# Optimization experiments

Measured on AMD Instinct MI355X. Metric: run time of the kernel, lower is better.

## Reference

```python
import jax, jax.numpy as jnp
import numpy as np


def setup_inputs() -> dict:
    key = jax.random.key(0)
    ks = jax.random.split(key, 4)
    B, C, H, W = 8, 512, 128, 128
    K, D = 150, 512
    std = 0.02
    return {
        "x": jax.random.normal(ks[0], (B, C, H, W), dtype=jnp.float32),
        "cls_repr": jax.random.normal(ks[1], (1, K, D), dtype=jnp.float32) * std,
        "W_cls": jax.random.normal(ks[2], (D, D), dtype=jnp.float32) * std,
        "W_feat": jax.random.normal(ks[3], (D, D), dtype=jnp.float32) * std,
        "ln_gamma": jnp.ones((K,), dtype=jnp.float32),
        "ln_beta": jnp.zeros((K,), dtype=jnp.float32),
    }


def reference(x, cls_repr, W_cls, W_feat, ln_gamma, ln_beta):
    b, c, h, w = x.shape
    K = cls_repr.shape[1]
    # img_feat: [b, hw, c]
    img_feat = jnp.transpose(x, (0, 2, 3, 1)).reshape(b, h * w, c)
    cls = jnp.broadcast_to(cls_repr, (b, K, c))
    # coupled_attn: [b, K, hw]
    coupled_attn = jnp.einsum("bnc,bkc->bkn", img_feat, cls)
    # class-direction softmax over hw, feeds class offsets
    cls_attn = jax.nn.softmax(coupled_attn, axis=2)                 # [b,K,hw]
    cls_offset = jnp.einsum("bkn,bnc->bkc", cls_attn, img_feat) @ W_cls.T
    aligned_cls = cls + cls_offset                                   # [b,K,c]
    # position-direction softmax over K, feeds feature offsets
    pos_attn = jax.nn.softmax(coupled_attn, axis=1)                 # [b,K,hw]
    feat_offset = jnp.einsum("bkn,bkc->bnc", pos_attn, cls) @ W_feat.T
    aligned_feat = img_feat + feat_offset                            # [b,hw,c]
    # masks: [b, hw, K], LayerNorm over K
    masks = jnp.einsum("bnc,bkc->bnk", aligned_feat, aligned_cls)
    mu = jnp.mean(masks, axis=-1, keepdims=True)
    var = jnp.var(masks, axis=-1, keepdims=True)
    masks = (masks - mu) * jax.lax.rsqrt(var + 1e-5) * ln_gamma + ln_beta
    return jnp.transpose(masks, (0, 2, 1)).reshape(b, K, h, w)
```

## Files before the change

### kernel.cpp

```cpp
#include <hip/hip_runtime.h>
#include <math.h>

#define BB 8
#define CC 512
#define HWN 16384
#define KK 150
#define KP 160
#define NSEG 16
#define SEGN (HWN / NSEG)

typedef short bf8v __attribute__((ext_vector_type(8)));
typedef float f4v __attribute__((ext_vector_type(4)));

static __device__ inline unsigned short f2b(float f) {
  unsigned u = __float_as_uint(f);
  u += 0x7fffu + ((u >> 16) & 1u);
  return (unsigned short)(u >> 16);
}
static __device__ inline float b2f(unsigned short s) {
  return __uint_as_float(((unsigned)s) << 16);
}
static __device__ inline float b2fs(short s) { return b2f((unsigned short)s); }

typedef const __attribute__((address_space(1))) void* gas_p;
typedef __attribute__((address_space(3))) void* las_p;
static __device__ __forceinline__ void gload16(const void* gp, void* lp) {
  __builtin_amdgcn_global_load_lds((gas_p)gp, (las_p)lp, 16, 0, 0);
}

__global__ __launch_bounds__(256) void t0_prep(const float* __restrict__ cls,
                                               const float* __restrict__ Wc,
                                               const float* __restrict__ Wf,
                                               unsigned short* __restrict__ cls16,
                                               unsigned short* __restrict__ Wc16,
                                               unsigned short* __restrict__ Wf16,
                                               unsigned short* __restrict__ MT16,
                                               unsigned short* __restrict__ AC16) {
  int i = blockIdx.x * 256 + threadIdx.x;
  if (i < KP * CC) {
    int k = i >> 9, c = i & 511;
    cls16[i] = (k < KK) ? f2b(cls[k * CC + c]) : 0;
  }
  if (i < BB * KP * KP) MT16[i] = 0;
  if (i < BB * (KP - KK) * CC) {
    int b = i / ((KP - KK) * CC);
    int r = i % ((KP - KK) * CC);
    int k = KK + (r >> 9);
    int c = r & 511;
    AC16[((size_t)b * KP + k) * CC + c] = 0;
  }
  if (i < CC * CC) {
    Wc16[i] = f2b(Wc[i]);
    Wf16[i] = f2b(Wf[i]);
  }
}

__global__ __launch_bounds__(256) void t1_transpose(const float* __restrict__ x,
                                                    unsigned short* __restrict__ xT,
                                                    unsigned short* __restrict__ x16) {
  __shared__ float ts[32][65];
  const int n0 = blockIdx.x * 64, c0 = blockIdx.y * 32, b = blockIdx.z;
  const int tid = threadIdx.x;
  const float* xb = x + (size_t)b * CC * HWN;
  unsigned short* x16o = x16 + (size_t)b * CC * HWN;
#pragma unroll
  for (int i = 0; i < 2; i++) {
    int e = tid + i * 256;
    int c = e >> 4, n4 = (e & 15) * 4;
    float4 v = *(const float4*)&xb[(size_t)(c0 + c) * HWN + n0 + n4];
    ts[c][n4] = v.x;
    ts[c][n4 + 1] = v.y;
    ts[c][n4 + 2] = v.z;
    ts[c][n4 + 3] = v.w;
    ushort4 pk;
    pk.x = f2b(v.x);
    pk.y = f2b(v.y);
    pk.z = f2b(v.z);
    pk.w = f2b(v.w);
    *(ushort4*)&x16o[(size_t)(c0 + c) * HWN + n0 + n4] = pk;
  }
  __syncthreads();
  unsigned short* xo = xT + (size_t)b * HWN * CC;
#pragma unroll
  for (int i = 0; i < 2; i++) {
    int e = tid + i * 256;
    int cg = e & 7, n = e >> 3;
    ushort4 pk;
    pk.x = f2b(ts[4 * cg][n]);
    pk.y = f2b(ts[4 * cg + 1][n]);
    pk.z = f2b(ts[4 * cg + 2][n]);
    pk.w = f2b(ts[4 * cg + 3][n]);
    *(ushort4*)&xo[(size_t)(n0 + n) * CC + c0 + 4 * cg] = pk;
  }
}

__global__ __launch_bounds__(256) void g1_mfma(const unsigned short* __restrict__ xT,
                                               const unsigned short* __restrict__ cls16,
                                               unsigned short* __restrict__ E16,
                                               unsigned short* __restrict__ ET16,
                                               float* __restrict__ vvec) {
  __shared__ unsigned short sA[2][KP * 32];
  __shared__ unsigned short sB[2][128 * 32];
  const int n0 = blockIdx.x * 128, b = blockIdx.y;
  const int tid = threadIdx.x, w = tid >> 6, L = tid & 63;
  const int q = L >> 4, m16 = L & 15;
  f4v zf = {0.f, 0.f, 0.f, 0.f};
  f4v acc[10][2];
#pragma unroll
  for (int mt = 0; mt < 10; mt++) { acc[mt][0] = zf; acc[mt][1] = zf; }
  const unsigned short* xbase = xT + (size_t)(b * HWN + n0) * CC;
  const int lr = L >> 2, lch = L & 3;

#define G1_STAGE(buf, c0)                                                      \
  {                                                                            \
                \
    _Pragma("unroll") for (int j = 0; j < 2; j++) {                            \
      int row = w * 32 + j * 16 + lr;                                          \
      int ch = lch ^ ((row >> 1) & 3);                                         \
      gload16(xbase + (size_t)row * CC + (c0) + ch * 8,                        \
              &sB[buf][(w * 32 + j * 16) * 32]);                               \
    }                                                                          \
            \
    for (int i = w; i < 10; i += 4) {                                          \
      int row = 16 * i + lr;                                                   \
      int ch = lch ^ ((row >> 1) & 3);                                         \
      gload16(cls16 + (size_t)row * CC + (c0) + ch * 8, &sA[buf][i * 512]);    \
    }                                                                          \
  }

  G1_STAGE(0, 0);
  __syncthreads();
  const int br0 = w * 32 + m16, br1 = br0 + 16;
  const int bs0 = (q ^ ((br0 >> 1) & 3)) * 8, bs1 = (q ^ ((br1 >> 1) & 3)) * 8;
  for (int s = 0; s < 16; s++) {
    if (s < 15) G1_STAGE((s + 1) & 1, (s + 1) * 32);
    const int cur = s & 1;
    bf8v b0 = *(const bf8v*)&sB[cur][br0 * 32 + bs0];
    bf8v b1 = *(const bf8v*)&sB[cur][br1 * 32 + bs1];
#pragma unroll
    for (int mt = 0; mt < 10; mt++) {
      int ar = 16 * mt + m16;
      bf8v a = *(const bf8v*)&sA[cur][ar * 32 + (q ^ ((ar >> 1) & 3)) * 8];
      acc[mt][0] = __builtin_amdgcn_mfma_f32_16x16x32_bf16(a, b0, acc[mt][0], 0, 0, 0);
      acc[mt][1] = __builtin_amdgcn_mfma_f32_16x16x32_bf16(a, b1, acc[mt][1], 0, 0, 0);
    }
    __syncthreads();
  }
  float cs0 = 0.f, cs1 = 0.f;
#pragma unroll
  for (int mt = 0; mt < 10; mt++)
#pragma unroll
    for (int r = 0; r < 4; r++) {
      int k = 16 * mt + 4 * q + r;
      bool valid = k < KK;
      float e0 = valid ? __expf(acc[mt][0][r]) : 0.f;
      float e1 = valid ? __expf(acc[mt][1][r]) : 0.f;
      acc[mt][0][r] = e0;
      acc[mt][1][r] = e1;
      cs0 += e0;
      cs1 += e1;
    }
#pragma unroll
  for (int mt = 0; mt < 10; mt++)
#pragma unroll
    for (int r = 0; r < 4; r++) {
      int k = 16 * mt + 4 * q + r;
      size_t row = ((size_t)(b * KP + k)) * HWN + n0 + 32 * w;
      E16[row + m16] = f2b(acc[mt][0][r]);
      E16[row + 16 + m16] = f2b(acc[mt][1][r]);
    }
  const int nA = n0 + 32 * w + m16;
#pragma unroll
  for (int mt = 0; mt < 10; mt++) {
    unsigned lo0 = (unsigned)f2b(acc[mt][0][0]) | ((unsigned)f2b(acc[mt][0][1]) << 16);
    unsigned hi0 = (unsigned)f2b(acc[mt][0][2]) | ((unsigned)f2b(acc[mt][0][3]) << 16);
    unsigned lo1 = (unsigned)f2b(acc[mt][1][0]) | ((unsigned)f2b(acc[mt][1][1]) << 16);
    unsigned hi1 = (unsigned)f2b(acc[mt][1][2]) | ((unsigned)f2b(acc[mt][1][3]) << 16);
    size_t eoff = ((size_t)(b * HWN + nA)) * KP + 16 * mt + 4 * q;
    *(uint2*)&ET16[eoff] = make_uint2(lo0, hi0);
    *(uint2*)&ET16[eoff + (size_t)16 * KP] = make_uint2(lo1, hi1);
  }
  cs0 += __shfl_xor(cs0, 16, 64);
  cs0 += __shfl_xor(cs0, 32, 64);
  cs1 += __shfl_xor(cs1, 16, 64);
  cs1 += __shfl_xor(cs1, 32, 64);
  if (q == 0) {
    vvec[b * HWN + nA] = 1.0f / cs0;
    vvec[b * HWN + nA + 16] = 1.0f / cs1;
  }
}

__global__ __launch_bounds__(256) void g2_rowsum(const unsigned short* __restrict__ E16,
                                                 float* __restrict__ rowsum) {
  const int bk = blockIdx.x;
  const int b = bk / KK, k = bk % KK;
  const bf8v* row = (const bf8v*)(E16 + ((size_t)(b * KP + k)) * HWN);
  __shared__ float red[4];
  const int tid = threadIdx.x, lane = tid & 63, w = tid >> 6;
  float s = 0.f;
  for (int i = tid; i < HWN / 8; i += 256) {
    bf8v u = row[i];
#pragma unroll
    for (int j = 0; j < 8; j++) s += b2fs(u[j]);
  }
#pragma unroll
  for (int o = 32; o > 0; o >>= 1) s += __shfl_down(s, o, 64);
  if (lane == 0) red[w] = s;
  __syncthreads();
  if (tid == 0) rowsum[bk] = red[0] + red[1] + red[2] + red[3];
}

__global__ __launch_bounds__(256) void g3_mfma(const unsigned short* __restrict__ x16,
                                               const unsigned short* __restrict__ E16,
                                               float* __restrict__ Scp) {
  const int cblk = blockIdx.x, seg = blockIdx.y, b = blockIdx.z;
  const int tid = threadIdx.x, w = tid >> 6, L = tid & 63;
  const int q = L >> 4, m16 = L & 15;
  f4v zf = {0.f, 0.f, 0.f, 0.f};
  f4v acc[10][2];
#pragma unroll
  for (int mt = 0; mt < 10; mt++) { acc[mt][0] = zf; acc[mt][1] = zf; }
  const unsigned short* eb = E16 + ((size_t)(b * KP + m16)) * HWN + 8 * q;
  const unsigned short* xb = x16 + ((size_t)(b * CC + cblk * 128 + 32 * w + m16)) * HWN + 8 * q;
  const int ns0 = seg * SEGN;
#pragma unroll 2
  for (int nc0 = ns0; nc0 < ns0 + SEGN; nc0 += 32) {
    bf8v x0 = *(const bf8v*)(xb + nc0);
    bf8v x1 = *(const bf8v*)(xb + (size_t)16 * HWN + nc0);
#pragma unroll
    for (int mt = 0; mt < 10; mt++) {
      bf8v a = *(const bf8v*)(eb + (size_t)(16 * mt) * HWN + nc0);
      acc[mt][0] = __builtin_amdgcn_mfma_f32_16x16x32_bf16(a, x0, acc[mt][0], 0, 0, 0);
      acc[mt][1] = __builtin_amdgcn_mfma_f32_16x16x32_bf16(a, x1, acc[mt][1], 0, 0, 0);
    }
  }
#pragma unroll
  for (int mt = 0; mt < 10; mt++)
#pragma unroll
    for (int cc = 0; cc < 2; cc++)
#pragma unroll
      for (int r = 0; r < 4; r++) {
        int k = 16 * mt + 4 * q + r;
        if (k < KK) {
          int c = cblk * 128 + 32 * w + 16 * cc + m16;
          Scp[(((size_t)(b * NSEG + seg)) * KK + k) * CC + c] = acc[mt][cc][r];
        }
      }
}

__global__ __launch_bounds__(256) void g5_reduce(const float* __restrict__ Scp,
                                                 const float* __restrict__ rowsum,
                                                 unsigned short* __restrict__ Sc16) {
  const int bk = blockIdx.x;
  const int b = bk / KK, k = bk % KK;
  const float inv = 1.0f / rowsum[bk];
  for (int c = threadIdx.x; c < CC; c += 256) {
    float s = 0.f;
    for (int g = 0; g < NSEG; g++)
      s += Scp[(((size_t)(b * NSEG + g)) * KK + k) * CC + c];
    Sc16[((size_t)b * KP + k) * CC + c] = f2b(s * inv);
  }
}

__global__ __launch_bounds__(256) void g4b_cwf(const unsigned short* __restrict__ cls16,
                                               const unsigned short* __restrict__ Wf16,
                                               unsigned short* __restrict__ CWf16) {
  const int tid = threadIdx.x, w = tid >> 6, L = tid & 63;
  const int q = L >> 4, m16 = L & 15;
  const int j0 = blockIdx.x * 128 + 32 * w;
  f4v zf = {0.f, 0.f, 0.f, 0.f};
  f4v acc[10][2];
#pragma unroll
  for (int mt = 0; mt < 10; mt++) { acc[mt][0] = zf; acc[mt][1] = zf; }
  const unsigned short* ar = cls16 + (size_t)m16 * CC + 8 * q;
  const unsigned short* br = Wf16 + (size_t)(j0 + m16) * CC + 8 * q;
#pragma unroll 2
  for (int c0 = 0; c0 < CC; c0 += 32) {
    bf8v b0 = *(const bf8v*)(br + c0);
    bf8v b1 = *(const bf8v*)(br + (size_t)16 * CC + c0);
#pragma unroll
    for (int mt = 0; mt < 10; mt++) {
      bf8v a = *(const bf8v*)(ar + (size_t)(16 * mt) * CC + c0);
      acc[mt][0] = __builtin_amdgcn_mfma_f32_16x16x32_bf16(a, b0, acc[mt][0], 0, 0, 0);
      acc[mt][1] = __builtin_amdgcn_mfma_f32_16x16x32_bf16(a, b1, acc[mt][1], 0, 0, 0);
    }
  }
#pragma unroll
  for (int mt = 0; mt < 10; mt++)
#pragma unroll
    for (int nc = 0; nc < 2; nc++)
#pragma unroll
      for (int r = 0; r < 4; r++) {
        int k1 = 16 * mt + 4 * q + r;
        int j = j0 + 16 * nc + m16;
        CWf16[(size_t)k1 * CC + j] = f2b(acc[mt][nc][r]);
      }
}

__global__ __launch_bounds__(256) void g4a_ac(const unsigned short* __restrict__ Sc16,
                                              const unsigned short* __restrict__ Wc16,
                                              const float* __restrict__ cls,
                                              unsigned short* __restrict__ AC16) {
  const int b = blockIdx.y;
  const int tid = threadIdx.x, w = tid >> 6, L = tid & 63;
  const int q = L >> 4, m16 = L & 15;
  const int j0 = blockIdx.x * 128 + 32 * w;
  f4v zf = {0.f, 0.f, 0.f, 0.f};
  f4v acc[10][2];
#pragma unroll
  for (int mt = 0; mt < 10; mt++) { acc[mt][0] = zf; acc[mt][1] = zf; }
  const unsigned short* ar = Sc16 + ((size_t)b * KP + m16) * CC + 8 * q;
  const unsigned short* br = Wc16 + (size_t)(j0 + m16) * CC + 8 * q;
#pragma unroll 2
  for (int c0 = 0; c0 < CC; c0 += 32) {
    bf8v b0 = *(const bf8v*)(br + c0);
    bf8v b1 = *(const bf8v*)(br + (size_t)16 * CC + c0);
#pragma unroll
    for (int mt = 0; mt < 10; mt++) {
      bf8v a = *(const bf8v*)(ar + (size_t)(16 * mt) * CC + c0);
      acc[mt][0] = __builtin_amdgcn_mfma_f32_16x16x32_bf16(a, b0, acc[mt][0], 0, 0, 0);
      acc[mt][1] = __builtin_amdgcn_mfma_f32_16x16x32_bf16(a, b1, acc[mt][1], 0, 0, 0);
    }
  }
#pragma unroll
  for (int mt = 0; mt < 10; mt++)
#pragma unroll
    for (int nc = 0; nc < 2; nc++)
#pragma unroll
      for (int r = 0; r < 4; r++) {
        int k = 16 * mt + 4 * q + r;
        if (k < KK) {
          int j = j0 + 16 * nc + m16;
          AC16[((size_t)b * KP + k) * CC + j] = f2b(cls[k * CC + j] + acc[mt][nc][r]);
        }
      }
}

__global__ __launch_bounds__(256) void g4c_m(const unsigned short* __restrict__ AC16,
                                             const unsigned short* __restrict__ CWf16,
                                             unsigned short* __restrict__ MT16) {
  const int b = blockIdx.y;
  const int tid = threadIdx.x, w = tid >> 6, L = tid & 63;
  const int q = L >> 4, m16 = L & 15;
  const int k1t = blockIdx.x * 64 + 16 * w;
  f4v zf = {0.f, 0.f, 0.f, 0.f};
  f4v acc[10];
#pragma unroll
  for (int mt = 0; mt < 10; mt++) acc[mt] = zf;
  const unsigned short* ar = AC16 + ((size_t)b * KP + m16) * CC + 8 * q;
  const unsigned short* br = CWf16 + (size_t)(k1t + m16) * CC + 8 * q;
#pragma unroll 2
  for (int c0 = 0; c0 < CC; c0 += 32) {
    bf8v bb = *(const bf8v*)(br + c0);
#pragma unroll
    for (int mt = 0; mt < 10; mt++) {
      bf8v a = *(const bf8v*)(ar + (size_t)(16 * mt) * CC + c0);
      acc[mt] = __builtin_amdgcn_mfma_f32_16x16x32_bf16(a, bb, acc[mt], 0, 0, 0);
    }
  }
  const int k1 = k1t + m16;
#pragma unroll
  for (int mt = 0; mt < 10; mt++)
#pragma unroll
    for (int r = 0; r < 4; r++) {
      int k2 = 16 * mt + 4 * q + r;
      if (k1 < KK) MT16[((size_t)b * KP + k2) * KP + k1] = f2b(acc[mt][r]);
    }
}

__global__ __launch_bounds__(256) void g6_mfma(
    const unsigned short* __restrict__ xT, const unsigned short* __restrict__ ET,
    const float* __restrict__ vvec, const unsigned short* __restrict__ AC16,
    const unsigned short* __restrict__ MT16, const float* __restrict__ gamma,
    const float* __restrict__ beta, float* __restrict__ out) {
  __shared__ unsigned short sA[2][KP * 32];
  __shared__ unsigned short sB[2][128 * 32];
  const int n0 = blockIdx.x * 128, b = blockIdx.y;
  const int tid = threadIdx.x, w = tid >> 6, L = tid & 63;
  const int q = L >> 4, m16 = L & 15;
  f4v zf = {0.f, 0.f, 0.f, 0.f};
  f4v acc[10][2];
#pragma unroll
  for (int mt = 0; mt < 10; mt++) { acc[mt][0] = zf; acc[mt][1] = zf; }

  const unsigned short* xbase = xT + (size_t)(b * HWN + n0) * CC;
  const unsigned short* abase = AC16 + (size_t)b * KP * CC;
  const int lr = L >> 2, lch = L & 3;
#define G6_STAGE(buf, c0)                                                      \
  {                                                                            \
    _Pragma("unroll") for (int j = 0; j < 2; j++) {                            \
      int row = w * 32 + j * 16 + lr;                                          \
      int ch = lch ^ ((row >> 1) & 3);                                         \
      gload16(xbase + (size_t)row * CC + (c0) + ch * 8,                        \
              &sB[buf][(w * 32 + j * 16) * 32]);                               \
    }                                                                          \
    for (int i = w; i < 10; i += 4) {                                          \
      int row = 16 * i + lr;                                                   \
      int ch = lch ^ ((row >> 1) & 3);                                         \
      gload16(abase + (size_t)row * CC + (c0) + ch * 8, &sA[buf][i * 512]);    \
    }                                                                          \
  }
  G6_STAGE(0, 0);

  const unsigned short* et0 = ET + ((size_t)(b * HWN + n0 + 32 * w + m16)) * KP + 8 * q;
  const unsigned short* et1 = et0 + 16 * KP;
  const unsigned short* mb = MT16 + (size_t)b * KP * KP + (size_t)m16 * KP + 8 * q;
#pragma unroll
  for (int kc = 0; kc < KP; kc += 32) {
    bf8v b0 = *(const bf8v*)(et0 + kc);
    bf8v b1 = *(const bf8v*)(et1 + kc);
#pragma unroll
    for (int mt = 0; mt < 10; mt++) {
      bf8v a = *(const bf8v*)(mb + (size_t)(16 * mt) * KP + kc);
      acc[mt][0] = __builtin_amdgcn_mfma_f32_16x16x32_bf16(a, b0, acc[mt][0], 0, 0, 0);
      acc[mt][1] = __builtin_amdgcn_mfma_f32_16x16x32_bf16(a, b1, acc[mt][1], 0, 0, 0);
    }
  }
  const float v0 = vvec[b * HWN + n0 + 32 * w + m16];
  const float v1 = vvec[b * HWN + n0 + 32 * w + 16 + m16];
#pragma unroll
  for (int mt = 0; mt < 10; mt++)
#pragma unroll
    for (int r = 0; r < 4; r++) {
      acc[mt][0][r] *= v0;
      acc[mt][1][r] *= v1;
    }

  __syncthreads();
  const int br0 = w * 32 + m16, br1 = br0 + 16;
  const int bs0 = (q ^ ((br0 >> 1) & 3)) * 8, bs1 = (q ^ ((br1 >> 1) & 3)) * 8;
  for (int s = 0; s < 16; s++) {
    if (s < 15) G6_STAGE((s + 1) & 1, (s + 1) * 32);
    const int cur = s & 1;
    bf8v b0 = *(const bf8v*)&sB[cur][br0 * 32 + bs0];
    bf8v b1 = *(const bf8v*)&sB[cur][br1 * 32 + bs1];
#pragma unroll
    for (int mt = 0; mt < 10; mt++) {
      int ar = 16 * mt + m16;
      bf8v a = *(const bf8v*)&sA[cur][ar * 32 + (q ^ ((ar >> 1) & 3)) * 8];
      acc[mt][0] = __builtin_amdgcn_mfma_f32_16x16x32_bf16(a, b0, acc[mt][0], 0, 0, 0);
      acc[mt][1] = __builtin_amdgcn_mfma_f32_16x16x32_bf16(a, b1, acc[mt][1], 0, 0, 0);
    }
    __syncthreads();
  }

  float s1[2] = {0.f, 0.f}, s2[2] = {0.f, 0.f};
#pragma unroll
  for (int mt = 0; mt < 10; mt++)
#pragma unroll
    for (int r = 0; r < 4; r++)
#pragma unroll
      for (int nc = 0; nc < 2; nc++) {
        float a = acc[mt][nc][r];
        s1[nc] += a;
        s2[nc] += a * a;
      }
#pragma unroll
  for (int nc = 0; nc < 2; nc++) {
    s1[nc] += __shfl_xor(s1[nc], 16, 64);
    s1[nc] += __shfl_xor(s1[nc], 32, 64);
    s2[nc] += __shfl_xor(s2[nc], 16, 64);
    s2[nc] += __shfl_xor(s2[nc], 32, 64);
  }
  float mu[2], inv[2];
#pragma unroll
  for (int nc = 0; nc < 2; nc++) {
    mu[nc] = s1[nc] * (1.0f / KK);
    float var = s2[nc] * (1.0f / KK) - mu[nc] * mu[nc];
    inv[nc] = rsqrtf(var + 1e-5f);
  }
#pragma unroll
  for (int mt = 0; mt < 10; mt++)
#pragma unroll
    for (int r = 0; r < 4; r++) {
      int k = 16 * mt + 4 * q + r;
      if (k < KK) {
        float g = gamma[k], be = beta[k];
        size_t row = (size_t)(b * KK + k) * HWN + n0 + 32 * w;
        out[row + m16] = (acc[mt][0][r] - mu[0]) * inv[0] * g + be;
        out[row + 16 + m16] = (acc[mt][1][r] - mu[1]) * inv[1] * g + be;
      }
    }
}

extern "C" void kernel_launch(void* const* d_in, const int* in_sizes, int n_in,
                              void* d_out, int out_size, void* d_ws, size_t ws_size,
                              hipStream_t stream) {
  const float* x = (const float*)d_in[0];
  const float* cls = (const float*)d_in[1];
  const float* Wc = (const float*)d_in[2];
  const float* Wf = (const float*)d_in[3];
  const float* gam = (const float*)d_in[4];
  const float* bet = (const float*)d_in[5];
  float* out = (float*)d_out;

  char* p = (char*)d_ws;
  auto alloc = [&](size_t bytes) {
    char* r = p;
    p += (bytes + 255) & ~(size_t)255;
    return r;
  };
  unsigned short* xT16 = (unsigned short*)alloc((size_t)BB * HWN * CC * 2);
  unsigned short* x16 = (unsigned short*)alloc((size_t)BB * CC * HWN * 2);
  unsigned short* E16 = (unsigned short*)alloc((size_t)BB * KP * HWN * 2);
  unsigned short* ET16 = (unsigned short*)alloc((size_t)BB * HWN * KP * 2);
  float* Scp = (float*)alloc((size_t)BB * NSEG * KK * CC * 4);
  unsigned short* Sc16 = (unsigned short*)alloc((size_t)BB * KP * CC * 2);
  unsigned short* AC16 = (unsigned short*)alloc((size_t)BB * KP * CC * 2);
  unsigned short* CWf16 = (unsigned short*)alloc((size_t)192 * CC * 2);
  unsigned short* cls16 = (unsigned short*)alloc((size_t)KP * CC * 2);
  unsigned short* Wc16 = (unsigned short*)alloc((size_t)CC * CC * 2);
  unsigned short* Wf16 = (unsigned short*)alloc((size_t)CC * CC * 2);
  unsigned short* MT16 = (unsigned short*)alloc((size_t)BB * KP * KP * 2);
  float* rowsum = (float*)alloc(BB * KK * 4);
  float* vvec = (float*)alloc((size_t)BB * HWN * 4);

  t0_prep<<<dim3((CC * CC + 255) / 256), 256, 0, stream>>>(cls, Wc, Wf, cls16, Wc16,
                                                           Wf16, MT16, AC16);
  t1_transpose<<<dim3(HWN / 64, CC / 32, BB), 256, 0, stream>>>(x, xT16, x16);
  g1_mfma<<<dim3(HWN / 128, BB), 256, 0, stream>>>(xT16, cls16, E16, ET16, vvec);
  g2_rowsum<<<dim3(BB * KK), 256, 0, stream>>>(E16, rowsum);
  g4b_cwf<<<dim3(CC / 128), 256, 0, stream>>>(cls16, Wf16, CWf16);
  g3_mfma<<<dim3(CC / 128, NSEG, BB), 256, 0, stream>>>(x16, E16, Scp);
  g5_reduce<<<dim3(BB * KK), 256, 0, stream>>>(Scp, rowsum, Sc16);
  g4a_ac<<<dim3(CC / 128, BB), 256, 0, stream>>>(Sc16, Wc16, cls, AC16);
  g4c_m<<<dim3(3, BB), 256, 0, stream>>>(AC16, CWf16, MT16);
  g6_mfma<<<dim3(HWN / 128, BB), 256, 0, stream>>>(xT16, ET16, vvec, AC16, MT16,
                                                   gam, bet, out);
}
```

Measured before the change: 820.6 us.

## Stage g3 GEMM operands through double-buffered swizzled LDS instead of direct global loads

The g3_mfma kernel previously had each wave load its E and x fragments straight from global memory, so all four waves re-fetched the same E rows. It now uses asynchronous global-to-LDS copies into double-buffered, XOR-swizzled shared tiles, as g1 already does, and reads the MFMA operands from LDS. The intent is to share the E tile across waves and overlap the next stage's loads with compute. In exchange it adds a block barrier per 32-element step and uses more LDS, which may lower occupancy.

```diff
diff --git a/kernel.cpp b/kernel.cpp
--- a/kernel.cpp
+++ b/kernel.cpp
@@ -113,14 +113,12 @@
 
 #define G1_STAGE(buf, c0)                                                      \
   {                                                                            \
-                \
     _Pragma("unroll") for (int j = 0; j < 2; j++) {                            \
       int row = w * 32 + j * 16 + lr;                                          \
       int ch = lch ^ ((row >> 1) & 3);                                         \
       gload16(xbase + (size_t)row * CC + (c0) + ch * 8,                        \
               &sB[buf][(w * 32 + j * 16) * 32]);                               \
     }                                                                          \
-            \
     for (int i = w; i < 10; i += 4) {                                          \
       int row = 16 * i + lr;                                                   \
       int ch = lch ^ ((row >> 1) & 3);                                         \
@@ -213,6 +211,8 @@
 __global__ __launch_bounds__(256) void g3_mfma(const unsigned short* __restrict__ x16,
                                                const unsigned short* __restrict__ E16,
                                                float* __restrict__ Scp) {
+  __shared__ unsigned short sA[2][KP * 32];
+  __shared__ unsigned short sB[2][128 * 32];
   const int cblk = blockIdx.x, seg = blockIdx.y, b = blockIdx.z;
   const int tid = threadIdx.x, w = tid >> 6, L = tid & 63;
   const int q = L >> 4, m16 = L & 15;
@@ -220,19 +220,42 @@
   f4v acc[10][2];
 #pragma unroll
   for (int mt = 0; mt < 10; mt++) { acc[mt][0] = zf; acc[mt][1] = zf; }
-  const unsigned short* eb = E16 + ((size_t)(b * KP + m16)) * HWN + 8 * q;
-  const unsigned short* xb = x16 + ((size_t)(b * CC + cblk * 128 + 32 * w + m16)) * HWN + 8 * q;
-  const int ns0 = seg * SEGN;
-#pragma unroll 2
-  for (int nc0 = ns0; nc0 < ns0 + SEGN; nc0 += 32) {
-    bf8v x0 = *(const bf8v*)(xb + nc0);
-    bf8v x1 = *(const bf8v*)(xb + (size_t)16 * HWN + nc0);
-#pragma unroll
-    for (int mt = 0; mt < 10; mt++) {
-      bf8v a = *(const bf8v*)(eb + (size_t)(16 * mt) * HWN + nc0);
-      acc[mt][0] = __builtin_amdgcn_mfma_f32_16x16x32_bf16(a, x0, acc[mt][0], 0, 0, 0);
-      acc[mt][1] = __builtin_amdgcn_mfma_f32_16x16x32_bf16(a, x1, acc[mt][1], 0, 0, 0);
-    }
+  const unsigned short* ebase = E16 + (size_t)(b * KP) * HWN + seg * SEGN;
+  const unsigned short* xbase = x16 + (size_t)(b * CC + cblk * 128) * HWN + seg * SEGN;
+  const int lr = L >> 2, lch = L & 3;
+
+#define G3_STAGE(buf, nof)                                                     \
+  {                                                                            \
+    _Pragma("unroll") for (int j = 0; j < 2; j++) {                            \
+      int row = w * 32 + j * 16 + lr;                                          \
+      int ch = lch ^ ((row >> 1) & 3);                                         \
+      gload16(xbase + (size_t)row * HWN + (nof) + ch * 8,                      \
+              &sB[buf][(w * 32 + j * 16) * 32]);                               \
+    }                                                                          \
+    for (int i = w; i < 10; i += 4) {                                          \
+      int row = 16 * i + lr;                                                   \
+      int ch = lch ^ ((row >> 1) & 3);                                         \
+      gload16(ebase + (size_t)row * HWN + (nof) + ch * 8, &sA[buf][i * 512]);  \
+    }                                                                          \
+  }
+
+  G3_STAGE(0, 0);
+  __syncthreads();
+  const int br0 = w * 32 + m16, br1 = br0 + 16;
+  const int bs0 = (q ^ ((br0 >> 1) & 3)) * 8, bs1 = (q ^ ((br1 >> 1) & 3)) * 8;
+  for (int s = 0; s < SEGN / 32; s++) {
+    if (s < SEGN / 32 - 1) G3_STAGE((s + 1) & 1, (s + 1) * 32);
+    const int cur = s & 1;
+    bf8v b0 = *(const bf8v*)&sB[cur][br0 * 32 + bs0];
+    bf8v b1 = *(const bf8v*)&sB[cur][br1 * 32 + bs1];
+#pragma unroll
+    for (int mt = 0; mt < 10; mt++) {
+      int ar = 16 * mt + m16;
+      bf8v a = *(const bf8v*)&sA[cur][ar * 32 + (q ^ ((ar >> 1) & 3)) * 8];
+      acc[mt][0] = __builtin_amdgcn_mfma_f32_16x16x32_bf16(a, b0, acc[mt][0], 0, 0, 0);
+      acc[mt][1] = __builtin_amdgcn_mfma_f32_16x16x32_bf16(a, b1, acc[mt][1], 0, 0, 0);
+    }
+    __syncthreads();
   }
 #pragma unroll
   for (int mt = 0; mt < 10; mt++)
```

New measurement: 783.0 us. 4.6% less time.
